# Kernel optimization log

Measured on AMD Instinct MI355X. Metric: run time of the kernel, lower is better.

Reference implementation:

```python
import jax, jax.numpy as jnp
import numpy as np

B, T, C, H = 8, 1024, 128, 8
BLOCK = 1024  # block_size; wpe has BLOCK+1 rows, last is padding (zeros)
E = C // H


def layer_norm(x, g, b, eps=1e-5):
    mu = jnp.mean(x, axis=-1, keepdims=True)
    var = jnp.var(x, axis=-1, keepdims=True)
    return (x - mu) * jax.lax.rsqrt(var + eps) * g + b


def setup_inputs() -> dict:
    key = jax.random.key(0)
    ks = jax.random.split(key, 7)
    x = jax.random.normal(ks[0], (B, T, C), dtype=jnp.float32)
    Wq = jax.random.normal(ks[1], (C, C), dtype=jnp.float32) * 0.02
    Wk = jax.random.normal(ks[2], (C, C), dtype=jnp.float32) * 0.02
    Wv = jax.random.normal(ks[3], (C, C), dtype=jnp.float32) * 0.02
    Wp = jax.random.normal(ks[4], (C, C), dtype=jnp.float32) * 0.02
    wpe = jax.random.normal(ks[5], (BLOCK + 1, C), dtype=jnp.float32) * 0.02
    wpe = wpe.at[BLOCK].set(0.0)  # padding_idx row is zero
    ln_g = jnp.ones((C,), dtype=jnp.float32)
    ln_b = jnp.zeros((C,), dtype=jnp.float32)
    return {"x": x, "Wq": Wq, "Wk": Wk, "Wv": Wv, "Wp": Wp,
            "wpe": wpe, "ln_g": ln_g, "ln_b": ln_b}


def reference(x, Wq, Wk, Wv, Wp, wpe, ln_g, ln_b):
    Bx, Tx, Cx = x.shape
    ln_x = layer_norm(x, ln_g, ln_b)
    # project and split heads: [B, H, T, E]
    q = (ln_x @ Wq).reshape(Bx, Tx, H, E).transpose(0, 2, 1, 3)
    k = (ln_x @ Wk).reshape(Bx, Tx, H, E).transpose(0, 2, 1, 3)
    v = (ln_x @ Wv).reshape(Bx, Tx, H, E).transpose(0, 2, 1, 3)
    # relative position indices: i-j, negatives -> padding row BLOCK
    i = jnp.arange(Tx)[:, None]
    j = jnp.arange(Tx)[None, :]
    rel_idx = jnp.where(i - j < 0, BLOCK, i - j)  # [T, T]
    rel = wpe[rel_idx].reshape(Tx, Tx, H, E)      # [T, T, H, E]
    scale = 1.0 / np.sqrt(E).astype(np.float32)
    scores = (jnp.einsum('bhte,bhse->bhts', q, k)
              + jnp.einsum('tshe,bhte->bhts', rel, q)) * scale
    causal = (j <= i)  # [T, T]
    scores = jnp.where(causal[None, None, :, :], scores, jnp.float32(-jnp.inf))
    attn = jax.nn.softmax(scores, axis=-1)
    y = jnp.einsum('bhts,bhse->bhte', attn, v)    # [B, H, T, E]
    y = y.transpose(0, 2, 1, 3).reshape(Bx, Tx, Cx)
    return y @ Wp + x
```

## Files before the change

### kernel.cpp

```cpp
#include <hip/hip_runtime.h>
#include <hip/hip_bf16.h>

#define B 8
#define T 1024
#define C 128
#define H 8
#define E 16
#define BH (B*H)
#define VSTR 17

typedef __attribute__((ext_vector_type(4)))  short bf16x4;
typedef __attribute__((ext_vector_type(8)))  short bf16x8;
typedef __attribute__((ext_vector_type(16))) float f32x16;

#define QSCALE 0.36067376022224085f

__device__ __forceinline__ unsigned short bfbits(float x) {
    __hip_bfloat16 h = __float2bfloat16(x);
    return __builtin_bit_cast(unsigned short, h);
}
__device__ __forceinline__ unsigned pack2(float a, float b) {
    return (unsigned)bfbits(a) | ((unsigned)bfbits(b) << 16);
}
__device__ __forceinline__ unsigned packtr(float a, float b) {
    return (__builtin_bit_cast(unsigned, a) >> 16) | (__builtin_bit_cast(unsigned, b) & 0xffff0000u);
}

__global__ __launch_bounds__(C) void k_prep(
    const float* __restrict__ wpe,
    const float* __restrict__ Wq, const float* __restrict__ Wk,
    const float* __restrict__ Wv, const float* __restrict__ Wp,
    __hip_bfloat16* __restrict__ Wpb,
    __hip_bfloat16* __restrict__ WT,
    __hip_bfloat16* __restrict__ WpT,
    ushort* __restrict__ VT)
{
    int bid = blockIdx.x, tid = threadIdx.x;
    if (bid < 1025) {
        int h = tid >> 4, e = tid & 15;
        Wpb[((size_t)h * 1025 + bid) * 16 + e] = __float2bfloat16(wpe[(size_t)bid * C + tid]);
    } else if (bid < 1537) {
        int n = bid - 1025;
        if (n < 128)      WT[n * C + tid]          = __float2bfloat16(Wq[tid * C + n] * QSCALE);
        else if (n < 256) WT[n * C + tid]          = __float2bfloat16(Wk[tid * C + (n - 128)]);
        else if (n < 384) WT[n * C + tid]          = __float2bfloat16(Wv[tid * C + (n - 256)]);
        else              WpT[(n - 384) * C + tid] = __float2bfloat16(Wp[tid * C + (n - 384)]);
    } else {
        int bh = bid - 1537;
        ushort* row = VT + ((size_t)bh * VSTR + 16) * T + tid * 8;
        uint2 ones = make_uint2(0x3F803F80u, 0x3F803F80u);
        *(uint2*)(row)     = ones;
        *(uint2*)(row + 4) = ones;
    }
}

__global__ __launch_bounds__(256) void k_qkv(
    const float* __restrict__ x, const float* __restrict__ g, const float* __restrict__ bb,
    const __hip_bfloat16* __restrict__ WT,
    __hip_bfloat16* __restrict__ Qb, __hip_bfloat16* __restrict__ Kb,
    __hip_bfloat16* __restrict__ VT)
{
    __shared__ ushort lnlds[32 * 132];
    const int tid = threadIdx.x;
    const int mt = blockIdx.x & 255, part = blockIdx.x >> 8;

    {
        const int r = tid >> 3, qq = tid & 7;
        const float* xp = x + ((size_t)mt * 32 + r) * C + qq * 16;
        float4 x0 = ((const float4*)xp)[0];
        float4 x1 = ((const float4*)xp)[1];
        float4 x2 = ((const float4*)xp)[2];
        float4 x3 = ((const float4*)xp)[3];
        float s1v = x0.x + x0.y + x0.z + x0.w + x1.x + x1.y + x1.z + x1.w
                  + x2.x + x2.y + x2.z + x2.w + x3.x + x3.y + x3.z + x3.w;
        float s2v = x0.x*x0.x + x0.y*x0.y + x0.z*x0.z + x0.w*x0.w
                  + x1.x*x1.x + x1.y*x1.y + x1.z*x1.z + x1.w*x1.w
                  + x2.x*x2.x + x2.y*x2.y + x2.z*x2.z + x2.w*x2.w
                  + x3.x*x3.x + x3.y*x3.y + x3.z*x3.z + x3.w*x3.w;
        s1v += __shfl_xor(s1v, 1, 64); s2v += __shfl_xor(s2v, 1, 64);
        s1v += __shfl_xor(s1v, 2, 64); s2v += __shfl_xor(s2v, 2, 64);
        s1v += __shfl_xor(s1v, 4, 64); s2v += __shfl_xor(s2v, 4, 64);
        float mu  = s1v * (1.f / C);
        float var = s2v * (1.f / C) - mu * mu;
        float rs  = rsqrtf(var + 1e-5f);
        const float4* gp = (const float4*)(g  + qq * 16);
        const float4* bp = (const float4*)(bb + qq * 16);
        float4 g0 = gp[0], g1 = gp[1], g2 = gp[2], g3 = gp[3];
        float4 b0 = bp[0], b1 = bp[1], b2 = bp[2], b3 = bp[3];
        #define LNV(xx, gg, bv) (((xx) - mu) * rs * (gg) + (bv))
        uint2* dst = (uint2*)&lnlds[r * 132 + qq * 16];
        dst[0] = make_uint2(pack2(LNV(x0.x,g0.x,b0.x), LNV(x0.y,g0.y,b0.y)),
                            pack2(LNV(x0.z,g0.z,b0.z), LNV(x0.w,g0.w,b0.w)));
        dst[1] = make_uint2(pack2(LNV(x1.x,g1.x,b1.x), LNV(x1.y,g1.y,b1.y)),
                            pack2(LNV(x1.z,g1.z,b1.z), LNV(x1.w,g1.w,b1.w)));
        dst[2] = make_uint2(pack2(LNV(x2.x,g2.x,b2.x), LNV(x2.y,g2.y,b2.y)),
                            pack2(LNV(x2.z,g2.z,b2.z), LNV(x2.w,g2.w,b2.w)));
        dst[3] = make_uint2(pack2(LNV(x3.x,g3.x,b3.x), LNV(x3.y,g3.y,b3.y)),
                            pack2(LNV(x3.z,g3.z,b3.z), LNV(x3.w,g3.w,b3.w)));
        #undef LNV
    }
    __syncthreads();

    const int wv = tid >> 6, lane = tid & 63, c = lane & 31, h5 = lane >> 5;
    const int b = mt >> 5, trow = (mt & 31) * 32;
    const int nt = part * 4 + wv, n0 = nt * 32;

    bf16x8 wf[8], lf[8];
    #pragma unroll
    for (int s = 0; s < 8; ++s)
        wf[s] = *(const bf16x8*)(WT + (size_t)(n0 + c) * C + 16 * s + 8 * h5);
    #pragma unroll
    for (int s = 0; s < 8; ++s) {
        const ushort* lp = &lnlds[c * 132 + 16 * s + 8 * h5];
        bf16x4 lo = *(const bf16x4*)lp;
        bf16x4 hi = *(const bf16x4*)(lp + 4);
        lf[s] = __builtin_shufflevector(lo, hi, 0, 1, 2, 3, 4, 5, 6, 7);
    }
    f32x16 acc;
    #pragma unroll
    for (int r = 0; r < 16; ++r) acc[r] = 0.f;

    if (nt < 8) {
        #pragma unroll
        for (int s = 0; s < 8; ++s)
            acc = __builtin_amdgcn_mfma_f32_32x32x16_bf16(wf[s], lf[s], acc, 0, 0, 0);
        __hip_bfloat16* base = (nt < 4) ? Qb : Kb;
        const int nb = (nt < 4 ? n0 : n0 - 128) + 4 * h5;
        #pragma unroll
        for (int j2 = 0; j2 < 4; ++j2) {
            int n = nb + 8 * j2;
            int h = n >> 4, e = n & 15;
            uint2 w = make_uint2(pack2(acc[4*j2], acc[4*j2+1]),
                                 pack2(acc[4*j2+2], acc[4*j2+3]));
            *(uint2*)(base + ((size_t)(b * H + h) * T + trow + c) * E + e) = w;
        }
    } else {
        #pragma unroll
        for (int s = 0; s < 8; ++s)
            acc = __builtin_amdgcn_mfma_f32_32x32x16_bf16(lf[s], wf[s], acc, 0, 0, 0);
        const int ecol = n0 - 256 + c;
        const int h = ecol >> 4, e = ecol & 15;
        __hip_bfloat16* vbase = VT + ((size_t)(b * H + h) * VSTR + e) * T + trow + 4 * h5;
        #pragma unroll
        for (int j2 = 0; j2 < 4; ++j2) {
            uint2 w = make_uint2(pack2(acc[4*j2], acc[4*j2+1]),
                                 pack2(acc[4*j2+2], acc[4*j2+3]));
            *(uint2*)(vbase + 8 * j2) = w;
        }
    }
}

__global__ __launch_bounds__(256) void k_attn(
    const __hip_bfloat16* __restrict__ Qb, const __hip_bfloat16* __restrict__ Kb,
    const __hip_bfloat16* __restrict__ VT, const __hip_bfloat16* __restrict__ Wpb,
    __hip_bfloat16* __restrict__ yb)
{
    __shared__ __align__(16) float U_all[4][32 * 68];
    __shared__ float mlb[4][2][32];

    const int tid = threadIdx.x, wv = tid >> 6, lane = tid & 63;
    const int h5 = lane >> 5, c = lane & 31;
    const int bh = blockIdx.x & 63;
    const int jq = 31 - (blockIdx.x >> 6);
    const int hh = bh & (H - 1);
    const int t0 = jq << 5;
    float* Uw = U_all[wv];

    const bf16x8 qf = *(const bf16x8*)(Qb + ((size_t)(bh * T + t0 + c) * E + 8 * h5));

    f32x16 Z, O;
    #pragma unroll
    for (int r = 0; r < 16; ++r) { Z[r] = 0.f; O[r] = 0.f; }
    float m = -1e30f;

    const bool hd   = ((jq & 3) == wv);
    const int nfull = (jq > wv) ? ((jq - wv + 3) >> 2) : 0;
    const int ntl   = nfull + (hd ? 1 : 0);

    const int s0w = 32 * wv;
    const bf16x8* kp  = (const bf16x8*)(Kb  + ((size_t)(bh * T + s0w + c) * E + 8 * h5));
    const bf16x8* wph = (const bf16x8*)(Wpb + ((size_t)(hh * 1025 + t0 - s0w + c) * E + 8 * h5));
    const bf16x8* wl0 = (const bf16x8*)(Wpb + ((size_t)hh * 1025 * E + 8 * h5));
    const ushort* vap = (const ushort*)(VT + ((size_t)(bh * VSTR + c) * T + s0w + 8 * h5));

    bf16x8 kf  = *kp;
    bf16x8 wfh = *wph;
    bf16x8 wfl = (hd && ntl == 1) ? *wl0 : *(const bf16x8*)((const ushort*)wph - 32 * E);

    for (int k = 0; k < ntl; ++k) {
        const bool diag = hd && (k == ntl - 1);

        const bf16x8 va = *(const bf16x8*)vap;
        const bf16x8 vb = *(const bf16x8*)(vap + 16);

        f32x16 S   = __builtin_amdgcn_mfma_f32_32x32x16_bf16(kf,  qf, Z, 0, 0, 0);
        f32x16 Ulo = __builtin_amdgcn_mfma_f32_32x32x16_bf16(wfl, qf, Z, 0, 0, 0);
        f32x16 Uhi = __builtin_amdgcn_mfma_f32_32x32x16_bf16(wfh, qf, Z, 0, 0, 0);

        float* up = Uw + c * 68 + 4 * h5;
        *(float4*)(up +  0) = make_float4(Ulo[0],  Ulo[1],  Ulo[2],  Ulo[3]);
        *(float4*)(up +  8) = make_float4(Ulo[4],  Ulo[5],  Ulo[6],  Ulo[7]);
        *(float4*)(up + 16) = make_float4(Ulo[8],  Ulo[9],  Ulo[10], Ulo[11]);
        *(float4*)(up + 24) = make_float4(Ulo[12], Ulo[13], Ulo[14], Ulo[15]);
        *(float4*)(up + 32) = make_float4(Uhi[0],  Uhi[1],  Uhi[2],  Uhi[3]);
        *(float4*)(up + 40) = make_float4(Uhi[4],  Uhi[5],  Uhi[6],  Uhi[7]);
        *(float4*)(up + 48) = make_float4(Uhi[8],  Uhi[9],  Uhi[10], Uhi[11]);
        *(float4*)(up + 56) = make_float4(Uhi[12], Uhi[13], Uhi[14], Uhi[15]);

        kp  = (const bf16x8*)((const ushort*)kp + 128 * E);
        wph = (const bf16x8*)((const ushort*)wph - 128 * E);
        vap += 128;
        const bool diag_next = hd && (k + 1 == ntl - 1);
        const bf16x8* wlp = diag_next ? wl0 : (const bf16x8*)((const ushort*)wph - 32 * E);
        bf16x8 nkf  = *kp;
        bf16x8 nwfh = *wph;
        bf16x8 nwfl = *wlp;

        const float* ur = Uw + c * 69 + 32 - 4 * h5;
        float sc[16];
        #pragma unroll
        for (int r = 0; r < 16; ++r)
            sc[r] = S[r] + ur[-((r & 3) + 8 * (r >> 2))];
        if (diag) {
            #pragma unroll
            for (int r = 0; r < 16; ++r) {
                const int rowm = 4 * h5 + (r & 3) + 8 * (r >> 2);
                sc[r] = (rowm <= c) ? sc[r] : -1e30f;
            }
        }
        float a0 = fmaxf(fmaxf(sc[0],  sc[1]),  sc[2]);
        float a1 = fmaxf(fmaxf(sc[3],  sc[4]),  sc[5]);
        float a2 = fmaxf(fmaxf(sc[6],  sc[7]),  sc[8]);
        float a3 = fmaxf(fmaxf(sc[9],  sc[10]), sc[11]);
        float a4 = fmaxf(fmaxf(sc[12], sc[13]), sc[14]);
        float pmax = fmaxf(fmaxf(fmaxf(a0, a1), sc[15]), fmaxf(fmaxf(a2, a3), a4));
        pmax = fmaxf(pmax, __shfl_xor(pmax, 32, 64));

        if (!__all(pmax <= m)) {
            const float mn = fmaxf(m, pmax);
            const float f = __builtin_amdgcn_exp2f(m - mn);
            #pragma unroll
            for (int r = 0; r < 9; ++r) O[r] *= f;
            m = mn;
        }
        float p[16];
        #pragma unroll
        for (int r = 0; r < 16; ++r) p[r] = __builtin_amdgcn_exp2f(sc[r] - m);

        unsigned w0 = packtr(p[0],  p[1]),  w1 = packtr(p[2],  p[3]);
        unsigned w2 = packtr(p[4],  p[5]),  w3 = packtr(p[6],  p[7]);
        unsigned w4 = packtr(p[8],  p[9]),  w5 = packtr(p[10], p[11]);
        unsigned w6 = packtr(p[12], p[13]), w7 = packtr(p[14], p[15]);
        unsigned r1 = __shfl_xor(h5 ? w0 : w2, 32, 64);
        unsigned r2 = __shfl_xor(h5 ? w1 : w3, 32, 64);
        unsigned r3 = __shfl_xor(h5 ? w4 : w6, 32, 64);
        unsigned r4 = __shfl_xor(h5 ? w5 : w7, 32, 64);
        uint4 f1 = h5 ? make_uint4(r1, r2, w2, w3) : make_uint4(w0, w1, r1, r2);
        uint4 f2 = h5 ? make_uint4(r3, r4, w6, w7) : make_uint4(w4, w5, r3, r4);
        bf16x8 pb1 = __builtin_bit_cast(bf16x8, f1);
        bf16x8 pb2 = __builtin_bit_cast(bf16x8, f2);

        O = __builtin_amdgcn_mfma_f32_32x32x16_bf16(va, pb1, O, 0, 0, 0);
        O = __builtin_amdgcn_mfma_f32_32x32x16_bf16(vb, pb2, O, 0, 0, 0);

        kf = nkf; wfh = nwfh; wfl = nwfl;
    }

    __syncthreads();
    float* Of = &U_all[0][0];
    if (h5 == 0) { mlb[wv][0][c] = m; mlb[wv][1][c] = O[8]; }
    float* ob = Of + (wv * 32 + c) * 16;
    *(float4*)(ob + 4 * h5)     = make_float4(O[0], O[1], O[2], O[3]);
    *(float4*)(ob + 4 * h5 + 8) = make_float4(O[4], O[5], O[6], O[7]);
    __syncthreads();
    if (wv == 0) {
        float mx = -1e30f;
        #pragma unroll
        for (int w = 0; w < 4; ++w) mx = fmaxf(mx, mlb[w][0][c]);
        float lt = 0.f;
        float a0=0, a1=0, a2=0, a3=0, b0=0, b1=0, b2=0, b3=0;
        #pragma unroll
        for (int w = 0; w < 4; ++w) {
            float fw = __builtin_amdgcn_exp2f(mlb[w][0][c] - mx);
            lt += mlb[w][1][c] * fw;
            const float* op = Of + (w * 32 + c) * 16;
            float4 o1 = *(const float4*)(op + 4 * h5);
            float4 o2 = *(const float4*)(op + 4 * h5 + 8);
            a0 += o1.x * fw; a1 += o1.y * fw; a2 += o1.z * fw; a3 += o1.w * fw;
            b0 += o2.x * fw; b1 += o2.y * fw; b2 += o2.z * fw; b3 += o2.w * fw;
        }
        float inv = 1.f / lt;
        __hip_bfloat16* yp = yb + ((size_t)((bh >> 3) * T + t0 + c)) * C + (bh & 7) * E + 4 * h5;
        *(uint2*)yp       = make_uint2(pack2(a0 * inv, a1 * inv), pack2(a2 * inv, a3 * inv));
        *(uint2*)(yp + 8) = make_uint2(pack2(b0 * inv, b1 * inv), pack2(b2 * inv, b3 * inv));
    }
}

__global__ __launch_bounds__(256) void k_proj(
    const __hip_bfloat16* __restrict__ yb, const __hip_bfloat16* __restrict__ WpT,
    const float* __restrict__ x, float* __restrict__ out)
{
    __shared__ ushort ylds[32 * 132];
    const int tid = threadIdx.x;
    const size_t row0 = (size_t)blockIdx.x * 32;

    #pragma unroll
    for (int ch = 0; ch < 2; ++ch) {
        int idx = tid + ch * 256;
        int r = idx >> 4, c8 = (idx & 15) * 8;
        const ushort* src = (const ushort*)yb + (row0 + r) * C + c8;
        uint4 a = *(const uint4*)src;
        *(uint2*)&ylds[r * 132 + c8]     = make_uint2(a.x, a.y);
        *(uint2*)&ylds[r * 132 + c8 + 4] = make_uint2(a.z, a.w);
    }
    __syncthreads();

    const int wv = tid >> 6, lane = tid & 63, c = lane & 31, h5 = lane >> 5;
    const int n0 = wv * 32;
    bf16x8 wf[8], yf[8];
    #pragma unroll
    for (int s = 0; s < 8; ++s)
        wf[s] = *(const bf16x8*)(WpT + (size_t)(n0 + c) * C + 16 * s + 8 * h5);
    #pragma unroll
    for (int s = 0; s < 8; ++s) {
        const ushort* lp = &ylds[c * 132 + 16 * s + 8 * h5];
        bf16x4 lo = *(const bf16x4*)lp;
        bf16x4 hi = *(const bf16x4*)(lp + 4);
        yf[s] = __builtin_shufflevector(lo, hi, 0, 1, 2, 3, 4, 5, 6, 7);
    }
    f32x16 acc;
    #pragma unroll
    for (int r = 0; r < 16; ++r) acc[r] = 0.f;
    #pragma unroll
    for (int s = 0; s < 8; ++s)
        acc = __builtin_amdgcn_mfma_f32_32x32x16_bf16(wf[s], yf[s], acc, 0, 0, 0);

    const size_t rb = (row0 + c) * C;
    #pragma unroll
    for (int j2 = 0; j2 < 4; ++j2) {
        int n = n0 + 4 * h5 + 8 * j2;
        float4 xr = *(const float4*)(x + rb + n);
        float4 o  = make_float4(acc[4*j2] + xr.x, acc[4*j2+1] + xr.y,
                                acc[4*j2+2] + xr.z, acc[4*j2+3] + xr.w);
        *(float4*)(out + rb + n) = o;
    }
}

extern "C" void kernel_launch(void* const* d_in, const int* in_sizes, int n_in,
                              void* d_out, int out_size, void* d_ws, size_t ws_size,
                              hipStream_t stream) {
    const float* x   = (const float*)d_in[0];
    const float* Wq  = (const float*)d_in[1];
    const float* Wk  = (const float*)d_in[2];
    const float* Wv  = (const float*)d_in[3];
    const float* Wp  = (const float*)d_in[4];
    const float* wpe = (const float*)d_in[5];
    const float* g   = (const float*)d_in[6];
    const float* bb  = (const float*)d_in[7];
    float* out = (float*)d_out;

    ushort* w = (ushort*)d_ws;
    __hip_bfloat16* Qb  = (__hip_bfloat16*)(w);
    __hip_bfloat16* Kb  = (__hip_bfloat16*)(w + 1048576);
    __hip_bfloat16* VT  = (__hip_bfloat16*)(w + 2097152);
    __hip_bfloat16* Wpb = (__hip_bfloat16*)(w + 3244032);
    __hip_bfloat16* WT  = (__hip_bfloat16*)(w + 3375232);
    __hip_bfloat16* WpT = (__hip_bfloat16*)(w + 3424384);
    __hip_bfloat16* yb  = (__hip_bfloat16*)(w + 3440768);

    k_prep <<<1025 + 512 + 64, C, 0, stream>>>(wpe, Wq, Wk, Wv, Wp, Wpb, WT, WpT, (ushort*)VT);
    k_qkv  <<<768,  256, 0, stream>>>(x, g, bb, WT, Qb, Kb, VT);
    k_attn <<<2048, 256, 0, stream>>>(Qb, Kb, VT, Wpb, yb);
    k_proj <<<256,  256, 0, stream>>>(yb, WpT, x, out);
}
```

Measured before the change: 41.94 us.

## Process two key tiles per attention loop iteration with double-buffered U staging

The attention inner loop now handles two 32-key tiles per iteration. It issues six score MFMAs back to back, stores both relative-position tiles into separate LDS buffers, and does one combined max and rescale per pair. This aims to give the scheduler more independent MFMA and memory work and to halve the online-softmax rescale overhead. The costs are higher register pressure from 32 scores, extra V and K fragments live at once, double the LDS footprint, and a remainder path for an odd tile count.

```diff
diff --git a/kernel.cpp b/kernel.cpp
--- a/kernel.cpp
+++ b/kernel.cpp
@@ -155,7 +155,7 @@
     const __hip_bfloat16* __restrict__ VT, const __hip_bfloat16* __restrict__ Wpb,
     __hip_bfloat16* __restrict__ yb)
 {
-    __shared__ __align__(16) float U_all[4][32 * 68];
+    __shared__ __align__(16) float U_all[4][2][32 * 68];
     __shared__ float mlb[4][2][32];
 
     const int tid = threadIdx.x, wv = tid >> 6, lane = tid & 63;
@@ -164,7 +164,8 @@
     const int jq = 31 - (blockIdx.x >> 6);
     const int hh = bh & (H - 1);
     const int t0 = jq << 5;
-    float* Uw = U_all[wv];
+    float* Uw0 = U_all[wv][0];
+    float* Uw1 = U_all[wv][1];
 
     const bf16x8 qf = *(const bf16x8*)(Qb + ((size_t)(bh * T + t0 + c) * E + 8 * h5));
 
@@ -178,50 +179,145 @@
     const int ntl   = nfull + (hd ? 1 : 0);
 
     const int s0w = 32 * wv;
-    const bf16x8* kp  = (const bf16x8*)(Kb  + ((size_t)(bh * T + s0w + c) * E + 8 * h5));
-    const bf16x8* wph = (const bf16x8*)(Wpb + ((size_t)(hh * 1025 + t0 - s0w + c) * E + 8 * h5));
-    const bf16x8* wl0 = (const bf16x8*)(Wpb + ((size_t)hh * 1025 * E + 8 * h5));
-    const ushort* vap = (const ushort*)(VT + ((size_t)(bh * VSTR + c) * T + s0w + 8 * h5));
-
-    bf16x8 kf  = *kp;
-    bf16x8 wfh = *wph;
-    bf16x8 wfl = (hd && ntl == 1) ? *wl0 : *(const bf16x8*)((const ushort*)wph - 32 * E);
-
-    for (int k = 0; k < ntl; ++k) {
-        const bool diag = hd && (k == ntl - 1);
-
+    const ushort* kpn  = (const ushort*)(Kb  + ((size_t)(bh * T + s0w + c) * E + 8 * h5));
+    const ushort* wphn = (const ushort*)(Wpb + ((size_t)(hh * 1025 + t0 - s0w + c) * E + 8 * h5));
+    const bf16x8* wl0  = (const bf16x8*)(Wpb + ((size_t)hh * 1025 * E + 8 * h5));
+    const ushort* vap  = (const ushort*)(VT + ((size_t)(bh * VSTR + c) * T + s0w + 8 * h5));
+
+    bf16x8 kfA, wfhA, wflA, kfB, wfhB, wflB;
+    int nl = 0;
+
+    #define LOADF(kf_, wfh_, wfl_)                                                     \
+    {   kf_  = *(const bf16x8*)kpn;                                                    \
+        wfh_ = *(const bf16x8*)wphn;                                                   \
+        wfl_ = (hd && nl == ntl - 1) ? *wl0 : *(const bf16x8*)(wphn - 32 * E);         \
+        kpn += 128 * E; wphn -= 128 * E; ++nl;                                         \
+    }
+
+    if (ntl > 0) LOADF(kfA, wfhA, wflA);
+    if (ntl > 1) LOADF(kfB, wfhB, wflB);
+
+    #define USTORE(Uw_, Ulo_, Uhi_)                                                    \
+    {   float* up = Uw_ + c * 68 + 4 * h5;                                             \
+        *(float4*)(up +  0) = make_float4(Ulo_[0],  Ulo_[1],  Ulo_[2],  Ulo_[3]);      \
+        *(float4*)(up +  8) = make_float4(Ulo_[4],  Ulo_[5],  Ulo_[6],  Ulo_[7]);      \
+        *(float4*)(up + 16) = make_float4(Ulo_[8],  Ulo_[9],  Ulo_[10], Ulo_[11]);     \
+        *(float4*)(up + 24) = make_float4(Ulo_[12], Ulo_[13], Ulo_[14], Ulo_[15]);     \
+        *(float4*)(up + 32) = make_float4(Uhi_[0],  Uhi_[1],  Uhi_[2],  Uhi_[3]);      \
+        *(float4*)(up + 40) = make_float4(Uhi_[4],  Uhi_[5],  Uhi_[6],  Uhi_[7]);      \
+        *(float4*)(up + 48) = make_float4(Uhi_[8],  Uhi_[9],  Uhi_[10], Uhi_[11]);     \
+        *(float4*)(up + 56) = make_float4(Uhi_[12], Uhi_[13], Uhi_[14], Uhi_[15]);     \
+    }
+
+    #define PACKP(pp, off, pb1_, pb2_)                                                 \
+    {   unsigned w0 = packtr(pp[off+0],  pp[off+1]),  w1 = packtr(pp[off+2],  pp[off+3]);  \
+        unsigned w2 = packtr(pp[off+4],  pp[off+5]),  w3 = packtr(pp[off+6],  pp[off+7]);  \
+        unsigned w4 = packtr(pp[off+8],  pp[off+9]),  w5 = packtr(pp[off+10], pp[off+11]); \
+        unsigned w6 = packtr(pp[off+12], pp[off+13]), w7 = packtr(pp[off+14], pp[off+15]); \
+        unsigned r1 = __shfl_xor(h5 ? w0 : w2, 32, 64);                                \
+        unsigned r2 = __shfl_xor(h5 ? w1 : w3, 32, 64);                                \
+        unsigned r3 = __shfl_xor(h5 ? w4 : w6, 32, 64);                                \
+        unsigned r4 = __shfl_xor(h5 ? w5 : w7, 32, 64);                                \
+        uint4 f1 = h5 ? make_uint4(r1, r2, w2, w3) : make_uint4(w0, w1, r1, r2);       \
+        uint4 f2 = h5 ? make_uint4(r3, r4, w6, w7) : make_uint4(w4, w5, r3, r4);       \
+        pb1_ = __builtin_bit_cast(bf16x8, f1);                                         \
+        pb2_ = __builtin_bit_cast(bf16x8, f2);                                         \
+    }
+
+    int k = 0;
+    while (k + 1 < ntl) {
+        const bool diagB = hd && (k + 2 == ntl);
+
+        const bf16x8 vaA = *(const bf16x8*)vap;
+        const bf16x8 vbA = *(const bf16x8*)(vap + 16);
+        const bf16x8 vaB = *(const bf16x8*)(vap + 128);
+        const bf16x8 vbB = *(const bf16x8*)(vap + 144);
+        vap += 256;
+
+        f32x16 SA   = __builtin_amdgcn_mfma_f32_32x32x16_bf16(kfA,  qf, Z, 0, 0, 0);
+        f32x16 SB   = __builtin_amdgcn_mfma_f32_32x32x16_bf16(kfB,  qf, Z, 0, 0, 0);
+        f32x16 UloA = __builtin_amdgcn_mfma_f32_32x32x16_bf16(wflA, qf, Z, 0, 0, 0);
+        f32x16 UhiA = __builtin_amdgcn_mfma_f32_32x32x16_bf16(wfhA, qf, Z, 0, 0, 0);
+        f32x16 UloB = __builtin_amdgcn_mfma_f32_32x32x16_bf16(wflB, qf, Z, 0, 0, 0);
+        f32x16 UhiB = __builtin_amdgcn_mfma_f32_32x32x16_bf16(wfhB, qf, Z, 0, 0, 0);
+
+        USTORE(Uw0, UloA, UhiA);
+        USTORE(Uw1, UloB, UhiB);
+
+        if (nl < ntl) LOADF(kfA, wfhA, wflA);
+        if (nl < ntl) LOADF(kfB, wfhB, wflB);
+
+        const float* urA = Uw0 + c * 69 + 32 - 4 * h5;
+        const float* urB = Uw1 + c * 69 + 32 - 4 * h5;
+        float sc[32];
+        #pragma unroll
+        for (int r = 0; r < 16; ++r) {
+            sc[r]      = SA[r] + urA[-((r & 3) + 8 * (r >> 2))];
+            sc[16 + r] = SB[r] + urB[-((r & 3) + 8 * (r >> 2))];
+        }
+        if (diagB) {
+            #pragma unroll
+            for (int r = 0; r < 16; ++r) {
+                const int rowm = 4 * h5 + (r & 3) + 8 * (r >> 2);
+                sc[16 + r] = (rowm <= c) ? sc[16 + r] : -1e30f;
+            }
+        }
+        float t00 = fmaxf(fmaxf(sc[0],  sc[1]),  sc[2]);
+        float t01 = fmaxf(fmaxf(sc[3],  sc[4]),  sc[5]);
+        float t02 = fmaxf(fmaxf(sc[6],  sc[7]),  sc[8]);
+        float t03 = fmaxf(fmaxf(sc[9],  sc[10]), sc[11]);
+        float t04 = fmaxf(fmaxf(sc[12], sc[13]), sc[14]);
+        float t05 = fmaxf(fmaxf(sc[15], sc[16]), sc[17]);
+        float t06 = fmaxf(fmaxf(sc[18], sc[19]), sc[20]);
+        float t07 = fmaxf(fmaxf(sc[21], sc[22]), sc[23]);
+        float t08 = fmaxf(fmaxf(sc[24], sc[25]), sc[26]);
+        float t09 = fmaxf(fmaxf(sc[27], sc[28]), sc[29]);
+        float t10 = fmaxf(sc[30], sc[31]);
+        float u0 = fmaxf(fmaxf(t00, t01), t02);
+        float u1 = fmaxf(fmaxf(t03, t04), t05);
+        float u2 = fmaxf(fmaxf(t06, t07), t08);
+        float u3 = fmaxf(t09, t10);
+        float pmax = fmaxf(fmaxf(u0, u1), fmaxf(u2, u3));
+        pmax = fmaxf(pmax, __shfl_xor(pmax, 32, 64));
+
+        if (!__all(pmax <= m)) {
+            const float mn = fmaxf(m, pmax);
+            const float f = __builtin_amdgcn_exp2f(m - mn);
+            #pragma unroll
+            for (int r = 0; r < 9; ++r) O[r] *= f;
+            m = mn;
+        }
+        #pragma unroll
+        for (int r = 0; r < 32; ++r) sc[r] = __builtin_amdgcn_exp2f(sc[r] - m);
+
+        bf16x8 pb1A, pb2A, pb1B, pb2B;
+        PACKP(sc, 0,  pb1A, pb2A);
+        PACKP(sc, 16, pb1B, pb2B);
+
+        O = __builtin_amdgcn_mfma_f32_32x32x16_bf16(vaA, pb1A, O, 0, 0, 0);
+        O = __builtin_amdgcn_mfma_f32_32x32x16_bf16(vbA, pb2A, O, 0, 0, 0);
+        O = __builtin_amdgcn_mfma_f32_32x32x16_bf16(vaB, pb1B, O, 0, 0, 0);
+        O = __builtin_amdgcn_mfma_f32_32x32x16_bf16(vbB, pb2B, O, 0, 0, 0);
+
+        k += 2;
+    }
+
+    if (k < ntl) {
         const bf16x8 va = *(const bf16x8*)vap;
         const bf16x8 vb = *(const bf16x8*)(vap + 16);
 
-        f32x16 S   = __builtin_amdgcn_mfma_f32_32x32x16_bf16(kf,  qf, Z, 0, 0, 0);
-        f32x16 Ulo = __builtin_amdgcn_mfma_f32_32x32x16_bf16(wfl, qf, Z, 0, 0, 0);
-        f32x16 Uhi = __builtin_amdgcn_mfma_f32_32x32x16_bf16(wfh, qf, Z, 0, 0, 0);
-
-        float* up = Uw + c * 68 + 4 * h5;
-        *(float4*)(up +  0) = make_float4(Ulo[0],  Ulo[1],  Ulo[2],  Ulo[3]);
-        *(float4*)(up +  8) = make_float4(Ulo[4],  Ulo[5],  Ulo[6],  Ulo[7]);
-        *(float4*)(up + 16) = make_float4(Ulo[8],  Ulo[9],  Ulo[10], Ulo[11]);
-        *(float4*)(up + 24) = make_float4(Ulo[12], Ulo[13], Ulo[14], Ulo[15]);
-        *(float4*)(up + 32) = make_float4(Uhi[0],  Uhi[1],  Uhi[2],  Uhi[3]);
-        *(float4*)(up + 40) = make_float4(Uhi[4],  Uhi[5],  Uhi[6],  Uhi[7]);
-        *(float4*)(up + 48) = make_float4(Uhi[8],  Uhi[9],  Uhi[10], Uhi[11]);
-        *(float4*)(up + 56) = make_float4(Uhi[12], Uhi[13], Uhi[14], Uhi[15]);
-
-        kp  = (const bf16x8*)((const ushort*)kp + 128 * E);
-        wph = (const bf16x8*)((const ushort*)wph - 128 * E);
-        vap += 128;
-        const bool diag_next = hd && (k + 1 == ntl - 1);
-        const bf16x8* wlp = diag_next ? wl0 : (const bf16x8*)((const ushort*)wph - 32 * E);
-        bf16x8 nkf  = *kp;
-        bf16x8 nwfh = *wph;
-        bf16x8 nwfl = *wlp;
-
-        const float* ur = Uw + c * 69 + 32 - 4 * h5;
+        f32x16 S   = __builtin_amdgcn_mfma_f32_32x32x16_bf16(kfA,  qf, Z, 0, 0, 0);
+        f32x16 Ulo = __builtin_amdgcn_mfma_f32_32x32x16_bf16(wflA, qf, Z, 0, 0, 0);
+        f32x16 Uhi = __builtin_amdgcn_mfma_f32_32x32x16_bf16(wfhA, qf, Z, 0, 0, 0);
+
+        USTORE(Uw0, Ulo, Uhi);
+
+        const float* ur = Uw0 + c * 69 + 32 - 4 * h5;
         float sc[16];
         #pragma unroll
         for (int r = 0; r < 16; ++r)
             sc[r] = S[r] + ur[-((r & 3) + 8 * (r >> 2))];
-        if (diag) {
+        if (hd) {
             #pragma unroll
             for (int r = 0; r < 16; ++r) {
                 const int rowm = 4 * h5 + (r & 3) + 8 * (r >> 2);
@@ -243,31 +339,21 @@
             for (int r = 0; r < 9; ++r) O[r] *= f;
             m = mn;
         }
-        float p[16];
-        #pragma unroll
-        for (int r = 0; r < 16; ++r) p[r] = __builtin_amdgcn_exp2f(sc[r] - m);
-
-        unsigned w0 = packtr(p[0],  p[1]),  w1 = packtr(p[2],  p[3]);
-        unsigned w2 = packtr(p[4],  p[5]),  w3 = packtr(p[6],  p[7]);
-        unsigned w4 = packtr(p[8],  p[9]),  w5 = packtr(p[10], p[11]);
-        unsigned w6 = packtr(p[12], p[13]), w7 = packtr(p[14], p[15]);
-        unsigned r1 = __shfl_xor(h5 ? w0 : w2, 32, 64);
-        unsigned r2 = __shfl_xor(h5 ? w1 : w3, 32, 64);
-        unsigned r3 = __shfl_xor(h5 ? w4 : w6, 32, 64);
-        unsigned r4 = __shfl_xor(h5 ? w5 : w7, 32, 64);
-        uint4 f1 = h5 ? make_uint4(r1, r2, w2, w3) : make_uint4(w0, w1, r1, r2);
-        uint4 f2 = h5 ? make_uint4(r3, r4, w6, w7) : make_uint4(w4, w5, r3, r4);
-        bf16x8 pb1 = __builtin_bit_cast(bf16x8, f1);
-        bf16x8 pb2 = __builtin_bit_cast(bf16x8, f2);
+        #pragma unroll
+        for (int r = 0; r < 16; ++r) sc[r] = __builtin_amdgcn_exp2f(sc[r] - m);
+
+        bf16x8 pb1, pb2;
+        PACKP(sc, 0, pb1, pb2);
 
         O = __builtin_amdgcn_mfma_f32_32x32x16_bf16(va, pb1, O, 0, 0, 0);
         O = __builtin_amdgcn_mfma_f32_32x32x16_bf16(vb, pb2, O, 0, 0, 0);
-
-        kf = nkf; wfh = nwfh; wfl = nwfl;
-    }
+    }
+    #undef LOADF
+    #undef USTORE
+    #undef PACKP
 
     __syncthreads();
-    float* Of = &U_all[0][0];
+    float* Of = &U_all[0][0][0];
     if (h5 == 0) { mlb[wv][0][c] = m; mlb[wv][1][c] = O[8]; }
     float* ob = Of + (wv * 32 + c) * 16;
     *(float4*)(ob + 4 * h5)     = make_float4(O[0], O[1], O[2], O[3]);
```

Measured after the change: 45.02 us. 1.07x slower.
